# Performance work log

Hardware: AMD Instinct MI355X
Metric: run time of the kernel (lower is better)

The kernel has to match this reference:

```python
import jax, jax.numpy as jnp
import numpy as np
from jax.scipy.special import logsumexp

T = 2048   # trajectory length
S = 512    # state dim (self.s)
B = 16     # number of options (self.b)
A = 18     # number of actions (self.a)
PEN = 0.5  # abstract_penalty
NEG = -1e9 # padding log-prob for not-yet-created option rows


def setup_inputs() -> dict:
    key = jax.random.key(0)
    k1, k2, k3, k4, k5 = jax.random.split(key, 5)
    s_i = jax.random.normal(k1, (T + 1, S), dtype=jnp.float32)
    W_action = jax.random.normal(k2, (S, B * A), dtype=jnp.float32) * 0.05
    W_stop = jax.random.normal(k3, (S, B * 2), dtype=jnp.float32) * 0.05
    W_start = jax.random.normal(k4, (S, B), dtype=jnp.float32) * 0.05
    actions = jax.random.randint(k5, (T,), 0, A, dtype=jnp.int64)
    return {"s_i": s_i, "W_action": W_action, "W_stop": W_stop,
            "W_start": W_start, "actions": actions}


def _hmm_logp(s_i, W_action, W_stop, W_start, actions):
    # abstract_policy_net: linear heads + log_softmax over the relevant axis
    action_logps = jax.nn.log_softmax((s_i @ W_action).reshape(T + 1, B, A), axis=-1)
    stop_logps = jax.nn.log_softmax((s_i @ W_stop).reshape(T + 1, B, 2), axis=-1)
    start_logps = jax.nn.log_softmax(s_i @ W_start, axis=-1)  # (T+1, B)

    # padded option_step_dist buffer: row i is created at step i (torch.cat append)
    buf0 = jnp.full((T, B), NEG, dtype=s_i.dtype).at[0].set(start_logps[0])

    def step(carry, xs):
        buf, tot = carry
        i, act = xs
        stop = stop_logps[i]          # (B, 2)
        start_lps = start_logps[i]    # (B,)
        # rearrange mass: options that stop get redistributed to new starts
        total_rearrange = logsumexp(buf + stop[:, 1]) - PEN
        new_mass = start_lps + total_rearrange
        buf2 = (buf + stop[:, 0]).at[i].set(new_mass)
        buf = jnp.where(i > 0, buf2, buf)  # i == 0 skips the rearrange branch
        action_lps = action_logps[i, :, act]  # (B,)
        tot = tot + logsumexp(action_lps + buf)
        return (buf, tot), None

    xs = (jnp.arange(T), actions)
    (buf, total_logp), _ = jax.lax.scan(step, (buf0, jnp.asarray(0.0, s_i.dtype)), xs)
    # final: all options must stop (note original uses index 0 here, as in source)
    total_logp = total_logp + logsumexp(stop_logps[-1, :, 0] + buf)
    return total_logp


def reference(s_i, W_action, W_stop, W_start, actions):
    return _hmm_logp(s_i, W_action, W_stop, W_start, actions)
```

## Files before the change

### kernel.cpp

```cpp
#include <hip/hip_runtime.h>

#define TT    2048
#define SS    512
#define NB    16
#define EPEN  0.60653065971263342f
#define NCHUNK 64
#define CLEN   32

typedef __attribute__((ext_vector_type(4))) float  floatx4;
typedef __attribute__((ext_vector_type(8))) short  bf16x8;

__device__ __forceinline__ ushort f2bf(float x) {
  unsigned u = __float_as_uint(x);
  u += 0x7fffu + ((u >> 16) & 1u);
  return (ushort)(u >> 16);
}

__global__ __launch_bounds__(256) void prep_kernel(
    const float* __restrict__ Wa, const float* __restrict__ Ws,
    const float* __restrict__ Wst, ushort* __restrict__ Wt)
{
  int idx = blockIdx.x * 256 + threadIdx.x;
  if (idx >= 336 * 512) return;
  int col = idx >> 9, k = idx & 511;
  float v;
  if (col < 288)      v = Wa [(size_t)k * 288 + col];
  else if (col < 320) v = Ws [(size_t)k * 32  + (col - 288)];
  else                v = Wst[(size_t)k * 16  + (col - 320)];
  Wt[idx] = f2bf(v);
}

__global__ __launch_bounds__(512) void proj_kernel(
    const float* __restrict__ s_i,
    const ushort* __restrict__ Wt,
    const int*   __restrict__ actions,
    float4*      __restrict__ coef)
{
  __shared__ float lg[16][346];

  const int tid  = threadIdx.x;
  const int wave = tid >> 6, lane = tid & 63;
  const int q = lane >> 4, rc = lane & 15;
  const int row0 = blockIdx.x * 16;

  const int kh = wave >> 2;
  const int ng = wave & 3;
  const int ntiles = (ng == 0) ? 6 : 5;
  const int kt0 = kh * 8;

  int arow = row0 + rc; if (arow > TT) arow = TT;
  const float*  aRow  = s_i + (size_t)arow * SS + q * 8;
  const ushort* bBase = Wt + (size_t)rc * 512 + q * 8;

  floatx4 acc[6];
  #pragma unroll
  for (int j = 0; j < 6; ++j) acc[j] = (floatx4)(0.f);

  float4 a0C, a1C, a0N, a1N;
  bf16x8 bC[6], bN[6];

  a0C = *(const float4*)(aRow + kt0 * 32);
  a1C = *(const float4*)(aRow + kt0 * 32 + 4);
  #pragma unroll
  for (int j = 0; j < 6; ++j) {
    if (j < ntiles) {
      const int colt = ng + 4 * j;
      bC[j] = *(const bf16x8*)(bBase + (size_t)colt * (16 * 512) + kt0 * 32);
    }
  }

  #pragma unroll
  for (int kk = 0; kk < 8; ++kk) {
    const int kt = kt0 + kk;
    if (kk < 7) {
      a0N = *(const float4*)(aRow + (kt + 1) * 32);
      a1N = *(const float4*)(aRow + (kt + 1) * 32 + 4);
      #pragma unroll
      for (int j = 0; j < 6; ++j) {
        if (j < ntiles) {
          const int colt = ng + 4 * j;
          bN[j] = *(const bf16x8*)(bBase + (size_t)colt * (16 * 512) + (kt + 1) * 32);
        }
      }
    }
    bf16x8 af;
    af[0] = (short)f2bf(a0C.x); af[1] = (short)f2bf(a0C.y);
    af[2] = (short)f2bf(a0C.z); af[3] = (short)f2bf(a0C.w);
    af[4] = (short)f2bf(a1C.x); af[5] = (short)f2bf(a1C.y);
    af[6] = (short)f2bf(a1C.z); af[7] = (short)f2bf(a1C.w);
    #pragma unroll
    for (int j = 0; j < 6; ++j) {
      if (j < ntiles)
        acc[j] = __builtin_amdgcn_mfma_f32_16x16x32_bf16(af, bC[j], acc[j], 0, 0, 0);
    }
    a0C = a0N; a1C = a1N;
    #pragma unroll
    for (int j = 0; j < 6; ++j) {
      if (j < ntiles) bC[j] = bN[j];
    }
  }

  if (kh == 0) {
    #pragma unroll
    for (int j = 0; j < 6; ++j) {
      if (j < ntiles) {
        const int colt = ng + 4 * j;
        #pragma unroll
        for (int reg = 0; reg < 4; ++reg)
          lg[q * 4 + reg][colt * 16 + rc] = acc[j][reg];
      }
    }
  }
  __syncthreads();
  if (kh == 1) {
    #pragma unroll
    for (int j = 0; j < 6; ++j) {
      if (j < ntiles) {
        const int colt = ng + 4 * j;
        #pragma unroll
        for (int reg = 0; reg < 4; ++reg)
          lg[q * 4 + reg][colt * 16 + rc] += acc[j][reg];
      }
    }
  }
  __syncthreads();

  if (tid < 256) {
    const int r = tid >> 4, b = tid & 15;
    const int row = row0 + r;
    if (row < TT) {
      float m = -3.4e38f;
      #pragma unroll
      for (int a = 0; a < 18; ++a) m = fmaxf(m, lg[r][b * 18 + a]);
      float sum = 0.f;
      #pragma unroll
      for (int a = 0; a < 18; ++a) sum += __expf(lg[r][b * 18 + a] - m);
      int act = actions[row];
      float aprob = __expf(lg[r][b * 18 + act] - m) / sum;

      float x0 = lg[r][288 + 2 * b], x1 = lg[r][288 + 2 * b + 1];
      float mm = fmaxf(x0, x1);
      float e0 = __expf(x0 - mm), e1 = __expf(x1 - mm);
      float inv = 1.f / (e0 + e1);

      float ms = -3.4e38f;
      #pragma unroll
      for (int j = 0; j < 16; ++j) ms = fmaxf(ms, lg[r][320 + j]);
      float ssum = 0.f;
      #pragma unroll
      for (int j = 0; j < 16; ++j) ssum += __expf(lg[r][320 + j] - ms);
      float stp = __expf(lg[r][320 + b] - ms) / ssum;

      coef[(size_t)row * NB + b] = make_float4(e0 * inv, e1 * inv, stp, aprob);
    } else if (row == TT) {
      float x0 = lg[r][288 + 2 * b], x1 = lg[r][288 + 2 * b + 1];
      float mm = fmaxf(x0, x1);
      float e0 = __expf(x0 - mm), e1 = __expf(x1 - mm);
      coef[(size_t)TT * NB + b] = make_float4(1.f, 0.f, 0.f, e0 / (e0 + e1));
    }
  }
}

__global__ __launch_bounds__(64) void pass1_kernel(
    const float4* __restrict__ coef,
    float* __restrict__ Wws, float* __restrict__ Mws)
{
  const int chunk = blockIdx.x * 4 + (threadIdx.x >> 4);
  const int c = threadIdx.x & 15;
  const int i0 = chunk * CLEN + 1;

  float G[16];
  #pragma unroll
  for (int r = 0; r < 16; ++r) G[r] = (r == c) ? 1.f : 0.f;

  float4 cfA[16], cfB[16];
  #pragma unroll
  for (int r = 0; r < 16; ++r) cfA[r] = coef[(size_t)i0 * 16 + r];
  #pragma unroll
  for (int r = 0; r < 16; ++r) cfB[r] = coef[(size_t)(i0 + 1) * 16 + r];

#define P1BODY(CUR, NXT, J)                                                  \
  {                                                                          \
    if ((J) + 2 < CLEN) {                                                    \
      _Pragma("unroll")                                                      \
      for (int r = 0; r < 16; ++r)                                           \
        NXT[r] = coef[(size_t)(i0 + (J) + 2) * 16 + r];                      \
    }                                                                        \
    float ta = 0.f, tb = 0.f, tc = 0.f, td = 0.f;                            \
    _Pragma("unroll")                                                        \
    for (int r = 0; r < 4; ++r) {                                            \
      ta = fmaf(CUR[r].y,      G[r],      ta);                               \
      tb = fmaf(CUR[r + 4].y,  G[r + 4],  tb);                               \
      tc = fmaf(CUR[r + 8].y,  G[r + 8],  tc);                               \
      td = fmaf(CUR[r + 12].y, G[r + 12], td);                               \
    }                                                                        \
    float et = EPEN * ((ta + tb) + (tc + td));                               \
    _Pragma("unroll")                                                        \
    for (int r = 0; r < 16; ++r)                                             \
      G[r] = fmaf(CUR[r].x, G[r], CUR[r].z * et);                            \
    float wa = 0.f, wb = 0.f, wc = 0.f, wd = 0.f;                            \
    _Pragma("unroll")                                                        \
    for (int r = 0; r < 4; ++r) {                                            \
      wa = fmaf(CUR[r].w,      G[r],      wa);                               \
      wb = fmaf(CUR[r + 4].w,  G[r + 4],  wb);                               \
      wc = fmaf(CUR[r + 8].w,  G[r + 8],  wc);                               \
      wd = fmaf(CUR[r + 12].w, G[r + 12], wd);                               \
    }                                                                        \
    Wws[(size_t)(chunk * CLEN + (J)) * 16 + c] = (wa + wb) + (wc + wd);      \
  }

  for (int j = 0; j < CLEN; j += 2) {
    P1BODY(cfA, cfB, j);
    P1BODY(cfB, cfA, j + 1);
  }
#undef P1BODY

  #pragma unroll
  for (int r = 0; r < 16; ++r)
    Mws[chunk * 256 + r * 16 + c] = G[r];
}

__global__ __launch_bounds__(512) void pass2_kernel(
    const float4* __restrict__ coef,
    const float* __restrict__ Wws, const float* __restrict__ Mws,
    float* __restrict__ out)
{
  __shared__ float pbuf[NCHUNK][16];
  __shared__ float wacc[8];

  const int tid = threadIdx.x;
  long long Ktot = 0;

  if (tid < 64) {
    const int r = tid & 15, g = tid >> 4;
    float pj0 = coef[4 * g + 0].z;
    float pj1 = coef[4 * g + 1].z;
    float pj2 = coef[4 * g + 2].z;
    float pj3 = coef[4 * g + 3].z;

    const int moff = r * 16 + 4 * g;
    const int gb0 = (4 * g) * 4, gb1 = gb0 + 4, gb2 = gb0 + 8, gb3 = gb0 + 12;
    int Ecum = 0;

    float4 mR0 = *(const float4*)&Mws[0 * 256 + moff];
    float4 mR1 = *(const float4*)&Mws[1 * 256 + moff];
    float4 mR2 = *(const float4*)&Mws[2 * 256 + moff];
    float4 mR3 = *(const float4*)&Mws[3 * 256 + moff];
    float4 mR4 = *(const float4*)&Mws[4 * 256 + moff];
    float4 mR5 = *(const float4*)&Mws[5 * 256 + moff];
    float4 mR6 = *(const float4*)&Mws[6 * 256 + moff];
    float4 mR7 = *(const float4*)&Mws[7 * 256 + moff];

#define P2BODY(K, MREG, KPF)                                                 \
    {                                                                        \
      if (r == 0)                                                            \
        *(float4*)&pbuf[(K)][4 * g] = make_float4(pj0, pj1, pj2, pj3);       \
      Ktot += 32LL * (long long)Ecum;                                        \
      float part = fmaf(MREG.x, pj0,                                         \
                   fmaf(MREG.y, pj1, fmaf(MREG.z, pj2, MREG.w * pj3)));      \
      if ((KPF) < NCHUNK)                                                    \
        MREG = *(const float4*)&Mws[(KPF) * 256 + moff];                     \
      part += __int_as_float(                                                \
          __builtin_amdgcn_ds_swizzle(__float_as_int(part), 0x401F));        \
      int ip = __float_as_int(part);                                         \
      float n0 = __int_as_float(__builtin_amdgcn_ds_bpermute(gb0, ip)) +     \
                 __int_as_float(__builtin_amdgcn_ds_bpermute(gb0 + 128, ip));\
      float n1 = __int_as_float(__builtin_amdgcn_ds_bpermute(gb1, ip)) +     \
                 __int_as_float(__builtin_amdgcn_ds_bpermute(gb1 + 128, ip));\
      float n2 = __int_as_float(__builtin_amdgcn_ds_bpermute(gb2, ip)) +     \
                 __int_as_float(__builtin_amdgcn_ds_bpermute(gb2 + 128, ip));\
      float n3 = __int_as_float(__builtin_amdgcn_ds_bpermute(gb3, ip)) +     \
                 __int_as_float(__builtin_amdgcn_ds_bpermute(gb3 + 128, ip));\
      int y0b = __builtin_amdgcn_readfirstlane(__float_as_int(n0));          \
      int eb = (y0b >> 23) & 255;                                            \
      Ecum += eb - 127;                                                      \
      float sc = __int_as_float((254 - eb) << 23);                           \
      pj0 = n0 * sc; pj1 = n1 * sc; pj2 = n2 * sc; pj3 = n3 * sc;            \
    }

    for (int kb = 0; kb < NCHUNK; kb += 8) {
      P2BODY(kb + 0, mR0, kb + 8);
      P2BODY(kb + 1, mR1, kb + 9);
      P2BODY(kb + 2, mR2, kb + 10);
      P2BODY(kb + 3, mR3, kb + 11);
      P2BODY(kb + 4, mR4, kb + 12);
      P2BODY(kb + 5, mR5, kb + 13);
      P2BODY(kb + 6, mR6, kb + 14);
      P2BODY(kb + 7, mR7, kb + 15);
    }
#undef P2BODY
  }
  __syncthreads();

  const int j0 = tid * 4;
  const int chunk = j0 >> 5;
  float p[16];
  #pragma unroll
  for (int c = 0; c < 16; ++c) p[c] = pbuf[chunk][c];

  float lacc = 0.f;
  #pragma unroll
  for (int jj = 0; jj < 4; ++jj) {
    const float* w = Wws + (size_t)(j0 + jj) * 16;
    float4 w0 = *(const float4*)(w);
    float4 w1 = *(const float4*)(w + 4);
    float4 w2 = *(const float4*)(w + 8);
    float4 w3 = *(const float4*)(w + 12);
    float s0 = fmaf(w0.x, p[0],  fmaf(w0.y, p[1],  fmaf(w0.z, p[2],  w0.w * p[3])));
    float s1 = fmaf(w1.x, p[4],  fmaf(w1.y, p[5],  fmaf(w1.z, p[6],  w1.w * p[7])));
    float s2 = fmaf(w2.x, p[8],  fmaf(w2.y, p[9],  fmaf(w2.z, p[10], w2.w * p[11])));
    float s3 = fmaf(w3.x, p[12], fmaf(w3.y, p[13], fmaf(w3.z, p[14], w3.w * p[15])));
    lacc += __logf((s0 + s1) + (s2 + s3));
  }

  if (tid == 0) {
    float U0 = 0.f;
    #pragma unroll
    for (int c = 0; c < 16; ++c) U0 = fmaf(coef[c].w, coef[c].z, U0);
    lacc += __logf(U0);
  }

  lacc += __shfl_xor(lacc, 1, 64);
  lacc += __shfl_xor(lacc, 2, 64);
  lacc += __shfl_xor(lacc, 4, 64);
  lacc += __shfl_xor(lacc, 8, 64);
  lacc += __shfl_xor(lacc, 16, 64);
  lacc += __shfl_xor(lacc, 32, 64);
  if ((tid & 63) == 0) wacc[tid >> 6] = lacc;
  __syncthreads();
  if (tid == 0) {
    double s = 0.0;
    #pragma unroll
    for (int i = 0; i < 8; ++i) s += (double)wacc[i];
    out[0] = (float)(s + 0.6931471805599453 * (double)Ktot);
  }
}

extern "C" void kernel_launch(void* const* d_in, const int* in_sizes, int n_in,
                              void* d_out, int out_size, void* d_ws, size_t ws_size,
                              hipStream_t stream) {
  const float* s_i = (const float*)d_in[0];
  const float* Wa  = (const float*)d_in[1];
  const float* Ws  = (const float*)d_in[2];
  const float* Wst = (const float*)d_in[3];
  const int*   act = (const int*)d_in[4];

  char* ws = (char*)d_ws;
  float4* coef = (float4*)ws;
  float*  Wws  = (float*)(ws + 524544);
  float*  Mws  = (float*)(ws + 524544 + 131072);
  ushort* Wt   = (ushort*)(ws + 524544 + 131072 + 65536);

  prep_kernel <<<672, 256, 0, stream>>>(Wa, Ws, Wst, Wt);
  proj_kernel <<<129, 512, 0, stream>>>(s_i, Wt, act, coef);
  pass1_kernel<<<16,  64,  0, stream>>>(coef, Wws, Mws);
  pass2_kernel<<<1,   512, 0, stream>>>(coef, Wws, Mws, (float*)d_out);
}
```

Before: 106.7 us.

## Pre-convert activations to bf16 fragment layout and use DPP reductions in pass2

The prep kernel now writes both the weights and s_i in bf16, in a tiled layout that matches the MFMA fragments, so each lane of proj_kernel does a single 16-byte contiguous load per operand and no per-step f32-to-bf16 conversion. Pass2 remaps lanes so the cross-group sum is done with two DPP row rotations instead of a ds_swizzle and twice as many bpermutes, which shortens the serial chunk recurrence. The cost is an extra pass over s_i in prep and more workspace traffic.

```diff
diff --git a/kernel.cpp b/kernel.cpp
--- a/kernel.cpp
+++ b/kernel.cpp
@@ -16,23 +16,53 @@
   return (ushort)(u >> 16);
 }
 
+__device__ __forceinline__ unsigned pack2(ushort a, ushort b) {
+  return (unsigned)a | ((unsigned)b << 16);
+}
+
 __global__ __launch_bounds__(256) void prep_kernel(
     const float* __restrict__ Wa, const float* __restrict__ Ws,
-    const float* __restrict__ Wst, ushort* __restrict__ Wt)
+    const float* __restrict__ Wst, const float* __restrict__ s_i,
+    ushort* __restrict__ Wt2, ushort* __restrict__ Af)
 {
-  int idx = blockIdx.x * 256 + threadIdx.x;
-  if (idx >= 336 * 512) return;
-  int col = idx >> 9, k = idx & 511;
-  float v;
-  if (col < 288)      v = Wa [(size_t)k * 288 + col];
-  else if (col < 320) v = Ws [(size_t)k * 32  + (col - 288)];
-  else                v = Wst[(size_t)k * 16  + (col - 320)];
-  Wt[idx] = f2bf(v);
+  int fid = blockIdx.x * 256 + threadIdx.x;
+  if (fid < 21504) {
+    const int q = fid & 3, rc = (fid >> 2) & 15, kt = (fid >> 6) & 15, colt = fid >> 10;
+    const int col = colt * 16 + rc;
+    const int kbase = kt * 32 + q * 8;
+    ushort h[8];
+    #pragma unroll
+    for (int e = 0; e < 8; ++e) {
+      const int k = kbase + e;
+      float v;
+      if (col < 288)      v = Wa [(size_t)k * 288 + col];
+      else if (col < 320) v = Ws [(size_t)k * 32  + (col - 288)];
+      else                v = Wst[(size_t)k * 16  + (col - 320)];
+      h[e] = f2bf(v);
+    }
+    uint4 o = make_uint4(pack2(h[0], h[1]), pack2(h[2], h[3]),
+                         pack2(h[4], h[5]), pack2(h[6], h[7]));
+    *(uint4*)(Wt2 + (size_t)fid * 8) = o;
+  } else {
+    const int aid = fid - 21504;
+    if (aid < 132096) {
+      const int q = aid & 3, rc = (aid >> 2) & 15, kt = (aid >> 6) & 15, mt = aid >> 10;
+      int row = mt * 16 + rc; if (row > TT) row = TT;
+      const float* src = s_i + (size_t)row * SS + kt * 32 + q * 8;
+      float4 v0 = *(const float4*)src;
+      float4 v1 = *(const float4*)(src + 4);
+      uint4 o = make_uint4(pack2(f2bf(v0.x), f2bf(v0.y)),
+                           pack2(f2bf(v0.z), f2bf(v0.w)),
+                           pack2(f2bf(v1.x), f2bf(v1.y)),
+                           pack2(f2bf(v1.z), f2bf(v1.w)));
+      *(uint4*)(Af + (size_t)aid * 8) = o;
+    }
+  }
 }
 
 __global__ __launch_bounds__(512) void proj_kernel(
-    const float* __restrict__ s_i,
-    const ushort* __restrict__ Wt,
+    const ushort* __restrict__ Af,
+    const ushort* __restrict__ Wt2,
     const int*   __restrict__ actions,
     float4*      __restrict__ coef)
 {
@@ -48,24 +78,21 @@
   const int ntiles = (ng == 0) ? 6 : 5;
   const int kt0 = kh * 8;
 
-  int arow = row0 + rc; if (arow > TT) arow = TT;
-  const float*  aRow  = s_i + (size_t)arow * SS + q * 8;
-  const ushort* bBase = Wt + (size_t)rc * 512 + q * 8;
+  const ushort* aBase = Af  + (size_t)blockIdx.x * 8192 + rc * 32 + q * 8;
+  const ushort* bBase = Wt2 + rc * 32 + q * 8;
 
   floatx4 acc[6];
   #pragma unroll
   for (int j = 0; j < 6; ++j) acc[j] = (floatx4)(0.f);
 
-  float4 a0C, a1C, a0N, a1N;
-  bf16x8 bC[6], bN[6];
-
-  a0C = *(const float4*)(aRow + kt0 * 32);
-  a1C = *(const float4*)(aRow + kt0 * 32 + 4);
+  bf16x8 aC, aN, bC[6], bN[6];
+
+  aC = *(const bf16x8*)(aBase + kt0 * 512);
   #pragma unroll
   for (int j = 0; j < 6; ++j) {
     if (j < ntiles) {
       const int colt = ng + 4 * j;
-      bC[j] = *(const bf16x8*)(bBase + (size_t)colt * (16 * 512) + kt0 * 32);
+      bC[j] = *(const bf16x8*)(bBase + (size_t)colt * 8192 + kt0 * 512);
     }
   }
 
@@ -73,27 +100,21 @@
   for (int kk = 0; kk < 8; ++kk) {
     const int kt = kt0 + kk;
     if (kk < 7) {
-      a0N = *(const float4*)(aRow + (kt + 1) * 32);
-      a1N = *(const float4*)(aRow + (kt + 1) * 32 + 4);
+      aN = *(const bf16x8*)(aBase + (kt + 1) * 512);
       #pragma unroll
       for (int j = 0; j < 6; ++j) {
         if (j < ntiles) {
           const int colt = ng + 4 * j;
-          bN[j] = *(const bf16x8*)(bBase + (size_t)colt * (16 * 512) + (kt + 1) * 32);
+          bN[j] = *(const bf16x8*)(bBase + (size_t)colt * 8192 + (kt + 1) * 512);
         }
       }
     }
-    bf16x8 af;
-    af[0] = (short)f2bf(a0C.x); af[1] = (short)f2bf(a0C.y);
-    af[2] = (short)f2bf(a0C.z); af[3] = (short)f2bf(a0C.w);
-    af[4] = (short)f2bf(a1C.x); af[5] = (short)f2bf(a1C.y);
-    af[6] = (short)f2bf(a1C.z); af[7] = (short)f2bf(a1C.w);
     #pragma unroll
     for (int j = 0; j < 6; ++j) {
       if (j < ntiles)
-        acc[j] = __builtin_amdgcn_mfma_f32_16x16x32_bf16(af, bC[j], acc[j], 0, 0, 0);
-    }
-    a0C = a0N; a1C = a1N;
+        acc[j] = __builtin_amdgcn_mfma_f32_16x16x32_bf16(aC, bC[j], acc[j], 0, 0, 0);
+    }
+    aC = aN;
     #pragma unroll
     for (int j = 0; j < 6; ++j) {
       if (j < ntiles) bC[j] = bN[j];
@@ -232,14 +253,14 @@
   long long Ktot = 0;
 
   if (tid < 64) {
-    const int r = tid & 15, g = tid >> 4;
+    const int r = tid >> 2, g = tid & 3;
     float pj0 = coef[4 * g + 0].z;
     float pj1 = coef[4 * g + 1].z;
     float pj2 = coef[4 * g + 2].z;
     float pj3 = coef[4 * g + 3].z;
 
     const int moff = r * 16 + 4 * g;
-    const int gb0 = (4 * g) * 4, gb1 = gb0 + 4, gb2 = gb0 + 8, gb3 = gb0 + 12;
+    const int gb0 = 64 * g, gb1 = gb0 + 16, gb2 = gb0 + 32, gb3 = gb0 + 48;
     int Ecum = 0;
 
     float4 mR0 = *(const float4*)&Mws[0 * 256 + moff];
@@ -260,17 +281,16 @@
                    fmaf(MREG.y, pj1, fmaf(MREG.z, pj2, MREG.w * pj3)));      \
       if ((KPF) < NCHUNK)                                                    \
         MREG = *(const float4*)&Mws[(KPF) * 256 + moff];                     \
-      part += __int_as_float(                                                \
-          __builtin_amdgcn_ds_swizzle(__float_as_int(part), 0x401F));        \
+              \
+      part += __int_as_float(__builtin_amdgcn_mov_dpp(                       \
+          __float_as_int(part), 0x39, 0xF, 0xF, true));      \
+      part += __int_as_float(__builtin_amdgcn_mov_dpp(                       \
+          __float_as_int(part), 0x4E, 0xF, 0xF, true));      \
       int ip = __float_as_int(part);                                         \
-      float n0 = __int_as_float(__builtin_amdgcn_ds_bpermute(gb0, ip)) +     \
-                 __int_as_float(__builtin_amdgcn_ds_bpermute(gb0 + 128, ip));\
-      float n1 = __int_as_float(__builtin_amdgcn_ds_bpermute(gb1, ip)) +     \
-                 __int_as_float(__builtin_amdgcn_ds_bpermute(gb1 + 128, ip));\
-      float n2 = __int_as_float(__builtin_amdgcn_ds_bpermute(gb2, ip)) +     \
-                 __int_as_float(__builtin_amdgcn_ds_bpermute(gb2 + 128, ip));\
-      float n3 = __int_as_float(__builtin_amdgcn_ds_bpermute(gb3, ip)) +     \
-                 __int_as_float(__builtin_amdgcn_ds_bpermute(gb3 + 128, ip));\
+      float n0 = __int_as_float(__builtin_amdgcn_ds_bpermute(gb0, ip));      \
+      float n1 = __int_as_float(__builtin_amdgcn_ds_bpermute(gb1, ip));      \
+      float n2 = __int_as_float(__builtin_amdgcn_ds_bpermute(gb2, ip));      \
+      float n3 = __int_as_float(__builtin_amdgcn_ds_bpermute(gb3, ip));      \
       int y0b = __builtin_amdgcn_readfirstlane(__float_as_int(n0));          \
       int eb = (y0b >> 23) & 255;                                            \
       Ecum += eb - 127;                                                      \
@@ -349,10 +369,11 @@
   float4* coef = (float4*)ws;
   float*  Wws  = (float*)(ws + 524544);
   float*  Mws  = (float*)(ws + 524544 + 131072);
-  ushort* Wt   = (ushort*)(ws + 524544 + 131072 + 65536);
-
-  prep_kernel <<<672, 256, 0, stream>>>(Wa, Ws, Wst, Wt);
-  proj_kernel <<<129, 512, 0, stream>>>(s_i, Wt, act, coef);
+  ushort* Wt2  = (ushort*)(ws + 721152);
+  ushort* Af   = (ushort*)(ws + 1065216);
+
+  prep_kernel <<<600, 256, 0, stream>>>(Wa, Ws, Wst, s_i, Wt2, Af);
+  proj_kernel <<<129, 512, 0, stream>>>(Af, Wt2, act, coef);
   pass1_kernel<<<16,  64,  0, stream>>>(coef, Wws, Mws);
   pass2_kernel<<<1,   512, 0, stream>>>(coef, Wws, Mws, (float*)d_out);
 }
```

After: 98.11 us. -8.0%, faster.
